# Performance work log

Hardware: AMD Instinct MI355X
Metric: run time of the kernel (lower is better)

Reference implementation:

```python
import jax, jax.numpy as jnp
import numpy as np

N_NODES = 50000
N_EDGES = 600000
N_GRAPHS = 100
IN_DIM, HID, OUT = 128, 128, 64
K = 2  # DGL TAGConv default hop count


def setup_inputs() -> dict:
    key = jax.random.key(0)
    ks = jax.random.split(key, 8)
    x = jax.random.normal(ks[0], (N_NODES, IN_DIM), dtype=jnp.float32)
    src = jax.random.randint(ks[1], (N_EDGES,), 0, N_NODES)
    dst = jax.random.randint(ks[2], (N_EDGES,), 0, N_NODES)
    graph_id = jnp.sort(jax.random.randint(ks[3], (N_NODES,), 0, N_GRAPHS))
    # TAGConv lin: Linear(in_feats*(K+1), out_feats), stored as (in*(K+1), out)
    W1 = jax.random.normal(ks[4], (IN_DIM * (K + 1), HID), dtype=jnp.float32) / np.sqrt(IN_DIM * (K + 1))
    b1 = jnp.zeros((HID,), dtype=jnp.float32)
    W2 = jax.random.normal(ks[5], (HID * (K + 1), OUT), dtype=jnp.float32) / np.sqrt(HID * (K + 1))
    b2 = jnp.zeros((OUT,), dtype=jnp.float32)
    return {"x": x, "W1": W1, "b1": b1, "W2": W2, "b2": b2,
            "src": src, "dst": dst, "graph_id": graph_id}


def _tagconv(h, src, dst, norm, W, b):
    """DGL TAGConv: relu(concat_k (D^-1/2 A D^-1/2)^k h @ W + b), k=0..K."""
    feats = [h]
    cur = h
    for _ in range(K):
        cur = cur * norm[:, None]
        cur = jax.ops.segment_sum(cur[src], dst, num_segments=N_NODES)
        cur = cur * norm[:, None]
        feats.append(cur)
    out = jnp.concatenate(feats, axis=-1) @ W + b
    return jax.nn.relu(out)


def reference(x, W1, b1, W2, b2, src, dst, graph_id):
    # symmetric norm from in-degrees (clamped to 1), as in DGL TAGConv
    deg = jax.ops.segment_sum(jnp.ones_like(dst, dtype=x.dtype), dst, num_segments=N_NODES)
    norm = jnp.clip(deg, 1.0, None) ** -0.5
    h = _tagconv(x, src, dst, norm, W1, b1)
    h = _tagconv(h, src, dst, norm, W2, b2)
    # MaxPooling readout: per-graph max over nodes
    return jax.ops.segment_max(h, graph_id, num_segments=N_GRAPHS)
```

## Files before the change

kernel.cpp:

```cpp
#include <hip/hip_runtime.h>
#include <hip/hip_bf16.h>

#define N_NODES 50000
#define N_EDGES 600000
#define N_GRAPHS 100
#define M_PAD 50176
#define TSLICE ((size_t)M_PAD * 32)

typedef __bf16 bf16_t;
typedef __attribute__((ext_vector_type(8))) __bf16 bf16x8;
typedef __attribute__((ext_vector_type(4))) __bf16 bf16x4;
typedef __attribute__((ext_vector_type(2))) __bf16 bf16x2;
typedef __attribute__((ext_vector_type(4))) float f32x4;

__global__ void degk(const int* __restrict__ dst, int* __restrict__ deg,
                     int* __restrict__ rank, int n) {
    int i = blockIdx.x * 256 + threadIdx.x;
    if (i < n) rank[i] = atomicAdd(&deg[dst[i]], 1);
}

__global__ __launch_bounds__(1024) void scan1(const int* __restrict__ deg,
                                              int* __restrict__ row_off,
                                              int* __restrict__ partial,
                                              float* __restrict__ norm, int n) {
    __shared__ int buf[1024];
    int i = blockIdx.x * 1024 + threadIdx.x;
    int v = (i < n) ? deg[i] : 0;
    buf[threadIdx.x] = v;
    __syncthreads();
    for (int off = 1; off < 1024; off <<= 1) {
        int t = (threadIdx.x >= off) ? buf[threadIdx.x - off] : 0;
        __syncthreads();
        buf[threadIdx.x] += t;
        __syncthreads();
    }
    if (i < n) {
        row_off[i + 1] = buf[threadIdx.x];
        float d = fmaxf((float)v, 1.0f);
        norm[i] = 1.0f / sqrtf(d);
    }
    if (threadIdx.x == 1023) partial[blockIdx.x] = buf[1023];
}

__global__ __launch_bounds__(256) void scan3(int* __restrict__ row_off,
                                             const int* __restrict__ partial, int n) {
    int i = blockIdx.x * 256 + threadIdx.x;
    int c = (blockIdx.x * 256) >> 10;
    __shared__ int pre;
    if (threadIdx.x < 64) {
        int v = (threadIdx.x < c) ? partial[threadIdx.x] : 0;
        for (int off = 32; off; off >>= 1) v += __shfl_down(v, off, 64);
        if (threadIdx.x == 0) pre = v;
    }
    __syncthreads();
    if (i == 0) row_off[0] = 0;
    if (i < n) row_off[i + 1] += pre;
}

#define NPRE 6250
#define NSC  ((N_EDGES + 255) / 256)
#define NPW  ((384 * 192 + 255) / 256)
__global__ __launch_bounds__(256) void midk(const float* __restrict__ x,
                                            const float* __restrict__ norm,
                                            bf16_t* __restrict__ xb, bf16_t* __restrict__ xs,
                                            const int* __restrict__ src, const int* __restrict__ dst,
                                            const int* __restrict__ row_off,
                                            const int* __restrict__ rank,
                                            int* __restrict__ csr_src,
                                            const float* __restrict__ W1, bf16_t* __restrict__ Wp1,
                                            const float* __restrict__ W2, bf16_t* __restrict__ Wp2) {
    int b = blockIdx.x;
    if (b < NPRE) {
        int i = b * 256 + threadIdx.x;
        int node = i >> 5, c4 = i & 31;
        float4 v = *(const float4*)(x + (size_t)node * 128 + c4 * 4);
        float nd = norm[node];
        bf16x4 ob, os;
        ob[0] = (bf16_t)v.x; ob[1] = (bf16_t)v.y; ob[2] = (bf16_t)v.z; ob[3] = (bf16_t)v.w;
        os[0] = (bf16_t)(v.x * nd); os[1] = (bf16_t)(v.y * nd);
        os[2] = (bf16_t)(v.z * nd); os[3] = (bf16_t)(v.w * nd);
        size_t t = (size_t)(c4 >> 3) * TSLICE + (size_t)node * 32 + (c4 & 7) * 4;
        *(bf16x4*)(xb + t) = ob;
        *(bf16x4*)(xs + t) = os;
    } else if (b < NPRE + NSC) {
        int e = (b - NPRE) * 256 + threadIdx.x;
        if (e >= N_EDGES) return;
        int d = dst[e];
        csr_src[row_off[d] + rank[e]] = src[e];
    } else {
        int i = (b - NPRE - NSC) * 256 + threadIdx.x;
        const float* W; bf16_t* Wp; int N; int idx;
        if (i < 384 * 128)                 { W = W1; Wp = Wp1; N = 128; idx = i; }
        else if (i < 384 * 128 + 384 * 64) { W = W2; Wp = Wp2; N = 64;  idx = i - 384 * 128; }
        else return;
        int k = idx / N, n = idx - k * N;
        int kt = k >> 5, q = (k >> 3) & 3, j = k & 7;
        int nt = n >> 4, ln = n & 15;
        int lane = q * 16 + ln;
        Wp[(((size_t)kt * (N >> 4) + nt) * 64 + lane) * 8 + j] = (bf16_t)W[idx];
    }
}

template <bool SCALED>
__global__ __launch_bounds__(256) void spmm_xcd(const bf16_t* __restrict__ in,
                                                bf16_t* __restrict__ out_c,
                                                bf16_t* __restrict__ out_s,
                                                const float* __restrict__ norm,
                                                const int* __restrict__ row_off,
                                                const int* __restrict__ csr_src, int n) {
    int bid  = blockIdx.x;
    int xcd  = bid & 7;
    int tile = xcd >> 1;
    int sub  = bid >> 3;
    int grp  = threadIdx.x >> 2;
    int l    = threadIdx.x & 3;
    int node = (sub * 2 + (xcd & 1)) * 64 + grp;
    if (node >= n) return;
    int e0 = row_off[node], e1 = row_off[node + 1];
    const bf16_t* base = in + (size_t)tile * TSLICE + l * 8;
    float acc[8] = {};
    int e = e0;
    for (; e + 8 <= e1; e += 8) {
        int s0 = csr_src[e + 0];
        int s1 = csr_src[e + 1];
        int s2 = csr_src[e + 2];
        int s3 = csr_src[e + 3];
        int s4 = csr_src[e + 4];
        int s5 = csr_src[e + 5];
        int s6 = csr_src[e + 6];
        int s7 = csr_src[e + 7];
        bf16x8 v0 = *(const bf16x8*)(base + (size_t)s0 * 32);
        bf16x8 v1 = *(const bf16x8*)(base + (size_t)s1 * 32);
        bf16x8 v2 = *(const bf16x8*)(base + (size_t)s2 * 32);
        bf16x8 v3 = *(const bf16x8*)(base + (size_t)s3 * 32);
        bf16x8 v4 = *(const bf16x8*)(base + (size_t)s4 * 32);
        bf16x8 v5 = *(const bf16x8*)(base + (size_t)s5 * 32);
        bf16x8 v6 = *(const bf16x8*)(base + (size_t)s6 * 32);
        bf16x8 v7 = *(const bf16x8*)(base + (size_t)s7 * 32);
#pragma unroll
        for (int j = 0; j < 8; j++)
            acc[j] += (((float)v0[j] + (float)v1[j]) + ((float)v2[j] + (float)v3[j]))
                    + (((float)v4[j] + (float)v5[j]) + ((float)v6[j] + (float)v7[j]));
    }
    if (e + 4 <= e1) {
        int s0 = csr_src[e + 0];
        int s1 = csr_src[e + 1];
        int s2 = csr_src[e + 2];
        int s3 = csr_src[e + 3];
        bf16x8 v0 = *(const bf16x8*)(base + (size_t)s0 * 32);
        bf16x8 v1 = *(const bf16x8*)(base + (size_t)s1 * 32);
        bf16x8 v2 = *(const bf16x8*)(base + (size_t)s2 * 32);
        bf16x8 v3 = *(const bf16x8*)(base + (size_t)s3 * 32);
#pragma unroll
        for (int j = 0; j < 8; j++)
            acc[j] += ((float)v0[j] + (float)v1[j]) + ((float)v2[j] + (float)v3[j]);
        e += 4;
    }
    for (; e < e1; e++) {
        int s = csr_src[e];
        bf16x8 v = *(const bf16x8*)(base + (size_t)s * 32);
#pragma unroll
        for (int j = 0; j < 8; j++) acc[j] += (float)v[j];
    }
    float nd = norm[node];
    bf16x8 oc, os;
#pragma unroll
    for (int j = 0; j < 8; j++) {
        float c = acc[j] * nd;
        oc[j] = (bf16_t)c;
        os[j] = (bf16_t)(c * nd);
    }
    size_t t = (size_t)tile * TSLICE + (size_t)node * 32 + l * 8;
    *(bf16x8*)(out_c + t) = oc;
    if (SCALED) *(bf16x8*)(out_s + t) = os;
}

template <int NT, bool LAYER1>
__global__ __launch_bounds__(256) void gemm_mfma(const bf16_t* __restrict__ f0,
                                                 const bf16_t* __restrict__ f1,
                                                 const bf16_t* __restrict__ f2,
                                                 const bf16_t* __restrict__ Wp,
                                                 const float* __restrict__ bias,
                                                 const float* __restrict__ norm,
                                                 bf16_t* __restrict__ out_b,
                                                 bf16_t* __restrict__ out_s,
                                                 float* __restrict__ out_f, int M) {
    int wave = threadIdx.x >> 6;
    int lane = threadIdx.x & 63;
    int q = lane >> 4, ln = lane & 15;
    int row0 = blockIdx.x * 128 + wave * 32;

    f32x4 acc[2][NT] = {};
    const bf16_t* feats[3] = {f0, f1, f2};
    const bf16x8* Wf = (const bf16x8*)Wp;

#pragma unroll
    for (int kc = 0; kc < 12; kc++) {
        const bf16_t* A = feats[kc >> 2] + (size_t)(kc & 3) * TSLICE + q * 8;
        bf16x8 a0 = *(const bf16x8*)(A + (size_t)(row0 + ln) * 32);
        bf16x8 a1 = *(const bf16x8*)(A + (size_t)(row0 + 16 + ln) * 32);
        const bf16x8* Bp = Wf + (size_t)kc * NT * 64 + lane;
#pragma unroll
        for (int nt = 0; nt < NT; nt++) {
            bf16x8 b = Bp[nt * 64];
            acc[0][nt] = __builtin_amdgcn_mfma_f32_16x16x32_bf16(a0, b, acc[0][nt], 0, 0, 0);
            acc[1][nt] = __builtin_amdgcn_mfma_f32_16x16x32_bf16(a1, b, acc[1][nt], 0, 0, 0);
        }
    }

    float bv[NT];
#pragma unroll
    for (int nt = 0; nt < NT; nt++) bv[nt] = bias[nt * 16 + ln];

#pragma unroll
    for (int mt = 0; mt < 2; mt++) {
#pragma unroll
        for (int r = 0; r < 4; r++) {
            int row = row0 + mt * 16 + q * 4 + r;
            if (row >= M) continue;
            float nd = LAYER1 ? norm[row] : 0.f;
#pragma unroll
            for (int nt = 0; nt < NT; nt++) {
                float val = fmaxf(acc[mt][nt][r] + bv[nt], 0.f);
                if (LAYER1) {
                    size_t t = (size_t)(nt >> 1) * TSLICE + (size_t)row * 32 + (nt & 1) * 16 + ln;
                    out_b[t] = (bf16_t)val;
                    out_s[t] = (bf16_t)(val * nd);
                } else {
                    out_f[(size_t)row * 64 + nt * 16 + ln] = val;
                }
            }
        }
    }
}

__global__ __launch_bounds__(256) void maxpool2(const float* __restrict__ hF,
                                                const int* __restrict__ gid,
                                                unsigned int* __restrict__ out, int n) {
    int wave = threadIdx.x >> 6;
    int lane = threadIdx.x & 63;
    int n0 = blockIdx.x * 256 + wave * 64;
    if (n0 >= n) return;
    int n1 = min(n0 + 64, n);
    int cur = gid[n0];
    float m = 0.f;
    int i = n0;
    for (; i + 4 <= n1; i += 4) {
        int g0 = gid[i + 0], g1 = gid[i + 1], g2 = gid[i + 2], g3 = gid[i + 3];
        float v0 = hF[(size_t)(i + 0) * 64 + lane];
        float v1 = hF[(size_t)(i + 1) * 64 + lane];
        float v2 = hF[(size_t)(i + 2) * 64 + lane];
        float v3 = hF[(size_t)(i + 3) * 64 + lane];
        if (g0 != cur) { atomicMax(&out[cur * 64 + lane], __float_as_uint(m)); cur = g0; m = v0; } else m = fmaxf(m, v0);
        if (g1 != cur) { atomicMax(&out[cur * 64 + lane], __float_as_uint(m)); cur = g1; m = v1; } else m = fmaxf(m, v1);
        if (g2 != cur) { atomicMax(&out[cur * 64 + lane], __float_as_uint(m)); cur = g2; m = v2; } else m = fmaxf(m, v2);
        if (g3 != cur) { atomicMax(&out[cur * 64 + lane], __float_as_uint(m)); cur = g3; m = v3; } else m = fmaxf(m, v3);
    }
    for (; i < n1; i++) {
        int g = gid[i];
        float v = hF[(size_t)i * 64 + lane];
        if (g != cur) { atomicMax(&out[cur * 64 + lane], __float_as_uint(m)); cur = g; m = v; }
        else m = fmaxf(m, v);
    }
    atomicMax(&out[cur * 64 + lane], __float_as_uint(m));
}

extern "C" void kernel_launch(void* const* d_in, const int* in_sizes, int n_in,
                              void* d_out, int out_size, void* d_ws, size_t ws_size,
                              hipStream_t stream) {
    const float* x  = (const float*)d_in[0];
    const float* W1 = (const float*)d_in[1];
    const float* b1 = (const float*)d_in[2];
    const float* W2 = (const float*)d_in[3];
    const float* b2 = (const float*)d_in[4];
    const int* src  = (const int*)d_in[5];
    const int* dst  = (const int*)d_in[6];
    const int* gid  = (const int*)d_in[7];
    float* out = (float*)d_out;

    char* ws = (char*)d_ws;
    size_t off = 0;
    auto take = [&](size_t bytes) {
        void* p = ws + off;
        off = (off + bytes + 255) & ~(size_t)255;
        return p;
    };
    int* deg     = (int*)take((size_t)N_NODES * 4);
    size_t zero_bytes = off;
    float* norm  = (float*)take((size_t)N_NODES * 4);
    int* row_off = (int*)take((size_t)(N_NODES + 1) * 4);
    int* partial = (int*)take(64 * 4);
    int* rank    = (int*)take((size_t)N_EDGES * 4);
    int* csr_src = (int*)take((size_t)N_EDGES * 4);
    bf16_t* Wp1  = (bf16_t*)take((size_t)384 * 128 * 2);
    bf16_t* Wp2  = (bf16_t*)take((size_t)384 * 64 * 2);
    bf16_t* B0 = (bf16_t*)take((size_t)M_PAD * 128 * 2);
    bf16_t* B1 = (bf16_t*)take((size_t)M_PAD * 128 * 2);
    bf16_t* B2 = (bf16_t*)take((size_t)M_PAD * 128 * 2);
    bf16_t* B3 = (bf16_t*)take((size_t)M_PAD * 128 * 2);
    bf16_t* B4 = (bf16_t*)take((size_t)M_PAD * 128 * 2);
    bf16_t* B5 = (bf16_t*)take((size_t)M_PAD * 128 * 2);
    (void)ws_size; (void)in_sizes; (void)n_in; (void)out_size;

    hipMemsetAsync(d_ws, 0, zero_bytes, stream);
    hipMemsetAsync(d_out, 0, (size_t)N_GRAPHS * 64 * 4, stream);

    degk<<<(N_EDGES + 255) / 256, 256, 0, stream>>>(dst, deg, rank, N_EDGES);
    int nchunks = (N_NODES + 1023) / 1024;
    scan1<<<nchunks, 1024, 0, stream>>>(deg, row_off, partial, norm, N_NODES);
    scan3<<<(N_NODES + 255) / 256, 256, 0, stream>>>(row_off, partial, N_NODES);
    midk<<<NPRE + NSC + NPW, 256, 0, stream>>>(x, norm, B0, B1, src, dst, row_off, rank,
                                               csr_src, W1, Wp1, W2, Wp2);

    int spmm_grid = 8 * 391;
    int gemm_grid = M_PAD / 128;

    spmm_xcd<true><<<spmm_grid, 256, 0, stream>>>(B1, B2, B4, norm, row_off, csr_src, N_NODES);
    spmm_xcd<false><<<spmm_grid, 256, 0, stream>>>(B4, B3, nullptr, norm, row_off, csr_src, N_NODES);
    gemm_mfma<8, true><<<gemm_grid, 256, 0, stream>>>(B0, B2, B3, Wp1, b1, norm, B5, B1, nullptr, N_NODES);
    spmm_xcd<true><<<spmm_grid, 256, 0, stream>>>(B1, B2, B4, norm, row_off, csr_src, N_NODES);
    spmm_xcd<false><<<spmm_grid, 256, 0, stream>>>(B4, B3, nullptr, norm, row_off, csr_src, N_NODES);
    gemm_mfma<4, false><<<gemm_grid, 256, 0, stream>>>(B5, B2, B3, Wp2, b2, nullptr, nullptr, nullptr, (float*)B0, N_NODES);
    maxpool2<<<(N_NODES + 255) / 256, 256, 0, stream>>>((const float*)B0, gid, (unsigned int*)out, N_NODES);
}
```

Baseline: 281.8 us.

## Apply layer-2 weights before propagation and split SpMM edges across thread halves

Layer 2 is reordered to multiply h by W2 first, since A(hW) = (Ah)W. The first propagation then runs on 128 projected columns, and the second hop only on the 64 columns that need two hops. The 64-wide results are summed with bias and ReLU inside the pooling kernel, which shrinks the gather traffic in layer-2 SpMM. SpMM now splits each node's edges between two 4-lane halves with a predicated first batch of 8 loads and a shuffle reduction, and stores through nontemporal writes. The cost is extra workspace buffers and a different bf16 rounding order.

```diff
diff --git a/kernel.cpp b/kernel.cpp
--- a/kernel.cpp
+++ b/kernel.cpp
@@ -10,7 +10,6 @@
 typedef __bf16 bf16_t;
 typedef __attribute__((ext_vector_type(8))) __bf16 bf16x8;
 typedef __attribute__((ext_vector_type(4))) __bf16 bf16x4;
-typedef __attribute__((ext_vector_type(2))) __bf16 bf16x2;
 typedef __attribute__((ext_vector_type(4))) float f32x4;
 
 __global__ void degk(const int* __restrict__ dst, int* __restrict__ deg,
@@ -89,108 +88,97 @@
         csr_src[row_off[d] + rank[e]] = src[e];
     } else {
         int i = (b - NPRE - NSC) * 256 + threadIdx.x;
-        const float* W; bf16_t* Wp; int N; int idx;
-        if (i < 384 * 128)                 { W = W1; Wp = Wp1; N = 128; idx = i; }
-        else if (i < 384 * 128 + 384 * 64) { W = W2; Wp = Wp2; N = 64;  idx = i - 384 * 128; }
-        else return;
-        int k = idx / N, n = idx - k * N;
-        int kt = k >> 5, q = (k >> 3) & 3, j = k & 7;
-        int nt = n >> 4, ln = n & 15;
-        int lane = q * 16 + ln;
-        Wp[(((size_t)kt * (N >> 4) + nt) * 64 + lane) * 8 + j] = (bf16_t)W[idx];
-    }
-}
-
-template <bool SCALED>
-__global__ __launch_bounds__(256) void spmm_xcd(const bf16_t* __restrict__ in,
-                                                bf16_t* __restrict__ out_c,
-                                                bf16_t* __restrict__ out_s,
-                                                const float* __restrict__ norm,
-                                                const int* __restrict__ row_off,
-                                                const int* __restrict__ csr_src, int n) {
+        if (i < 384 * 128) {
+            int k = i >> 7, n = i & 127;
+            int kt = k >> 5, q = (k >> 3) & 3, j = k & 7;
+            int nt = n >> 4, ln = n & 15;
+            Wp1[(((size_t)kt * 8 + nt) * 64 + q * 16 + ln) * 8 + j] = (bf16_t)W1[i];
+        } else if (i < 384 * 128 + 384 * 64) {
+            int idx = i - 384 * 128;
+            int k384 = idx >> 6, n = idx & 63;
+            int blk = k384 >> 7, kk = k384 & 127;
+            int col = blk * 64 + n;
+            int kt = kk >> 5, q = (kk >> 3) & 3, j = kk & 7;
+            int nt = col >> 4, ln = col & 15;
+            Wp2[(((size_t)kt * 12 + nt) * 64 + q * 16 + ln) * 8 + j] = (bf16_t)W2[idx];
+        }
+    }
+}
+
+template <int TILES, bool SCALED>
+__global__ __launch_bounds__(256) void spmm8(const bf16_t* __restrict__ in,
+                                             bf16_t* __restrict__ out_c,
+                                             bf16_t* __restrict__ out_s,
+                                             const float* __restrict__ norm,
+                                             const int* __restrict__ row_off,
+                                             const int* __restrict__ csr, int n) {
+    constexpr int PARTS = 8 / TILES;
     int bid  = blockIdx.x;
     int xcd  = bid & 7;
-    int tile = xcd >> 1;
+    int tile = xcd / PARTS;
+    int part = xcd % PARTS;
     int sub  = bid >> 3;
-    int grp  = threadIdx.x >> 2;
+    int grp  = threadIdx.x >> 3;
+    int half = (threadIdx.x >> 2) & 1;
     int l    = threadIdx.x & 3;
-    int node = (sub * 2 + (xcd & 1)) * 64 + grp;
+    int node = (sub * PARTS + part) * 32 + grp;
     if (node >= n) return;
     int e0 = row_off[node], e1 = row_off[node + 1];
     const bf16_t* base = in + (size_t)tile * TSLICE + l * 8;
     float acc[8] = {};
-    int e = e0;
-    for (; e + 8 <= e1; e += 8) {
-        int s0 = csr_src[e + 0];
-        int s1 = csr_src[e + 1];
-        int s2 = csr_src[e + 2];
-        int s3 = csr_src[e + 3];
-        int s4 = csr_src[e + 4];
-        int s5 = csr_src[e + 5];
-        int s6 = csr_src[e + 6];
-        int s7 = csr_src[e + 7];
-        bf16x8 v0 = *(const bf16x8*)(base + (size_t)s0 * 32);
-        bf16x8 v1 = *(const bf16x8*)(base + (size_t)s1 * 32);
-        bf16x8 v2 = *(const bf16x8*)(base + (size_t)s2 * 32);
-        bf16x8 v3 = *(const bf16x8*)(base + (size_t)s3 * 32);
-        bf16x8 v4 = *(const bf16x8*)(base + (size_t)s4 * 32);
-        bf16x8 v5 = *(const bf16x8*)(base + (size_t)s5 * 32);
-        bf16x8 v6 = *(const bf16x8*)(base + (size_t)s6 * 32);
-        bf16x8 v7 = *(const bf16x8*)(base + (size_t)s7 * 32);
-#pragma unroll
-        for (int j = 0; j < 8; j++)
-            acc[j] += (((float)v0[j] + (float)v1[j]) + ((float)v2[j] + (float)v3[j]))
-                    + (((float)v4[j] + (float)v5[j]) + ((float)v6[j] + (float)v7[j]));
-    }
-    if (e + 4 <= e1) {
-        int s0 = csr_src[e + 0];
-        int s1 = csr_src[e + 1];
-        int s2 = csr_src[e + 2];
-        int s3 = csr_src[e + 3];
-        bf16x8 v0 = *(const bf16x8*)(base + (size_t)s0 * 32);
-        bf16x8 v1 = *(const bf16x8*)(base + (size_t)s1 * 32);
-        bf16x8 v2 = *(const bf16x8*)(base + (size_t)s2 * 32);
-        bf16x8 v3 = *(const bf16x8*)(base + (size_t)s3 * 32);
-#pragma unroll
-        for (int j = 0; j < 8; j++)
-            acc[j] += ((float)v0[j] + (float)v1[j]) + ((float)v2[j] + (float)v3[j]);
-        e += 4;
-    }
-    for (; e < e1; e++) {
-        int s = csr_src[e];
-        bf16x8 v = *(const bf16x8*)(base + (size_t)s * 32);
-#pragma unroll
-        for (int j = 0; j < 8; j++) acc[j] += (float)v[j];
-    }
+    if (e0 < e1) {
+        int be   = e0 + half;
+        int cnt  = (e1 - be + 1) >> 1;
+        int emax = e1 - 1;
+        int s[8];
+#pragma unroll
+        for (int k = 0; k < 8; k++) s[k] = csr[min(be + 2 * k, emax)];
+        bf16x8 v[8];
+#pragma unroll
+        for (int k = 0; k < 8; k++) v[k] = *(const bf16x8*)(base + (size_t)s[k] * 32);
+#pragma unroll
+        for (int k = 0; k < 8; k++) {
+            float wk = (k < cnt) ? 1.0f : 0.0f;
+#pragma unroll
+            for (int j = 0; j < 8; j++) acc[j] += wk * (float)v[k][j];
+        }
+        for (int e = be + 16; e < e1; e += 2) {
+            int ss = csr[e];
+            bf16x8 vv = *(const bf16x8*)(base + (size_t)ss * 32);
+#pragma unroll
+            for (int j = 0; j < 8; j++) acc[j] += (float)vv[j];
+        }
+    }
+#pragma unroll
+    for (int j = 0; j < 8; j++) acc[j] += __shfl_xor(acc[j], 4, 64);
     float nd = norm[node];
-    bf16x8 oc, os;
-#pragma unroll
-    for (int j = 0; j < 8; j++) {
-        float c = acc[j] * nd;
-        oc[j] = (bf16_t)c;
-        os[j] = (bf16_t)(c * nd);
-    }
     size_t t = (size_t)tile * TSLICE + (size_t)node * 32 + l * 8;
-    *(bf16x8*)(out_c + t) = oc;
-    if (SCALED) *(bf16x8*)(out_s + t) = os;
-}
-
-template <int NT, bool LAYER1>
-__global__ __launch_bounds__(256) void gemm_mfma(const bf16_t* __restrict__ f0,
-                                                 const bf16_t* __restrict__ f1,
-                                                 const bf16_t* __restrict__ f2,
-                                                 const bf16_t* __restrict__ Wp,
-                                                 const float* __restrict__ bias,
-                                                 const float* __restrict__ norm,
-                                                 bf16_t* __restrict__ out_b,
-                                                 bf16_t* __restrict__ out_s,
-                                                 float* __restrict__ out_f, int M) {
+    if (half == 0) {
+        bf16x8 oc;
+#pragma unroll
+        for (int j = 0; j < 8; j++) oc[j] = (bf16_t)(acc[j] * nd);
+        __builtin_nontemporal_store(oc, (bf16x8*)(out_c + t));
+    } else if (SCALED) {
+        float n2 = nd * nd;
+        bf16x8 os;
+#pragma unroll
+        for (int j = 0; j < 8; j++) os[j] = (bf16_t)(acc[j] * n2);
+        __builtin_nontemporal_store(os, (bf16x8*)(out_s + t));
+    }
+}
+
+__global__ __launch_bounds__(256) void gemm1k(const bf16_t* __restrict__ f0,
+                                              const bf16_t* __restrict__ f1,
+                                              const bf16_t* __restrict__ f2,
+                                              const bf16_t* __restrict__ Wp,
+                                              const float* __restrict__ bias,
+                                              bf16_t* __restrict__ outb, int M) {
     int wave = threadIdx.x >> 6;
     int lane = threadIdx.x & 63;
     int q = lane >> 4, ln = lane & 15;
     int row0 = blockIdx.x * 128 + wave * 32;
 
-    f32x4 acc[2][NT] = {};
+    f32x4 acc[2][8] = {};
     const bf16_t* feats[3] = {f0, f1, f2};
     const bf16x8* Wf = (const bf16x8*)Wp;
 
@@ -199,18 +187,18 @@
         const bf16_t* A = feats[kc >> 2] + (size_t)(kc & 3) * TSLICE + q * 8;
         bf16x8 a0 = *(const bf16x8*)(A + (size_t)(row0 + ln) * 32);
         bf16x8 a1 = *(const bf16x8*)(A + (size_t)(row0 + 16 + ln) * 32);
-        const bf16x8* Bp = Wf + (size_t)kc * NT * 64 + lane;
-#pragma unroll
-        for (int nt = 0; nt < NT; nt++) {
+        const bf16x8* Bp = Wf + (size_t)kc * 8 * 64 + lane;
+#pragma unroll
+        for (int nt = 0; nt < 8; nt++) {
             bf16x8 b = Bp[nt * 64];
             acc[0][nt] = __builtin_amdgcn_mfma_f32_16x16x32_bf16(a0, b, acc[0][nt], 0, 0, 0);
             acc[1][nt] = __builtin_amdgcn_mfma_f32_16x16x32_bf16(a1, b, acc[1][nt], 0, 0, 0);
         }
     }
 
-    float bv[NT];
-#pragma unroll
-    for (int nt = 0; nt < NT; nt++) bv[nt] = bias[nt * 16 + ln];
+    float bv[8];
+#pragma unroll
+    for (int nt = 0; nt < 8; nt++) bv[nt] = bias[nt * 16 + ln];
 
 #pragma unroll
     for (int mt = 0; mt < 2; mt++) {
@@ -218,47 +206,86 @@
         for (int r = 0; r < 4; r++) {
             int row = row0 + mt * 16 + q * 4 + r;
             if (row >= M) continue;
-            float nd = LAYER1 ? norm[row] : 0.f;
-#pragma unroll
-            for (int nt = 0; nt < NT; nt++) {
+#pragma unroll
+            for (int nt = 0; nt < 8; nt++) {
                 float val = fmaxf(acc[mt][nt][r] + bv[nt], 0.f);
-                if (LAYER1) {
-                    size_t t = (size_t)(nt >> 1) * TSLICE + (size_t)row * 32 + (nt & 1) * 16 + ln;
-                    out_b[t] = (bf16_t)val;
-                    out_s[t] = (bf16_t)(val * nd);
-                } else {
-                    out_f[(size_t)row * 64 + nt * 16 + ln] = val;
-                }
+                outb[(size_t)(nt >> 1) * TSLICE + (size_t)row * 32 + (nt & 1) * 16 + ln] = (bf16_t)val;
             }
         }
     }
 }
 
-__global__ __launch_bounds__(256) void maxpool2(const float* __restrict__ hF,
-                                                const int* __restrict__ gid,
-                                                unsigned int* __restrict__ out, int n) {
+__global__ __launch_bounds__(256) void gemm2k(const bf16_t* __restrict__ h,
+                                              const bf16_t* __restrict__ Wp,
+                                              const float* __restrict__ bias,
+                                              const float* __restrict__ norm,
+                                              float* __restrict__ t0,
+                                              bf16_t* __restrict__ uvs, int M) {
+    int wave = threadIdx.x >> 6;
+    int lane = threadIdx.x & 63;
+    int q = lane >> 4, ln = lane & 15;
+    int row0 = blockIdx.x * 128 + wave * 32;
+
+    f32x4 acc[2][12] = {};
+    const bf16x8* Wf = (const bf16x8*)Wp;
+
+#pragma unroll
+    for (int kc = 0; kc < 4; kc++) {
+        const bf16_t* A = h + (size_t)kc * TSLICE + q * 8;
+        bf16x8 a0 = *(const bf16x8*)(A + (size_t)(row0 + ln) * 32);
+        bf16x8 a1 = *(const bf16x8*)(A + (size_t)(row0 + 16 + ln) * 32);
+        const bf16x8* Bp = Wf + (size_t)kc * 12 * 64 + lane;
+#pragma unroll
+        for (int nt = 0; nt < 12; nt++) {
+            bf16x8 b = Bp[nt * 64];
+            acc[0][nt] = __builtin_amdgcn_mfma_f32_16x16x32_bf16(a0, b, acc[0][nt], 0, 0, 0);
+            acc[1][nt] = __builtin_amdgcn_mfma_f32_16x16x32_bf16(a1, b, acc[1][nt], 0, 0, 0);
+        }
+    }
+
+    float bv[4];
+#pragma unroll
+    for (int nt = 0; nt < 4; nt++) bv[nt] = bias[nt * 16 + ln];
+
+#pragma unroll
+    for (int mt = 0; mt < 2; mt++) {
+#pragma unroll
+        for (int r = 0; r < 4; r++) {
+            int row = row0 + mt * 16 + q * 4 + r;
+            if (row >= M) continue;
+            float nd = norm[row];
+#pragma unroll
+            for (int nt = 0; nt < 4; nt++)
+                __builtin_nontemporal_store(acc[mt][nt][r] + bv[nt],
+                                            t0 + (size_t)row * 64 + nt * 16 + ln);
+#pragma unroll
+            for (int nt = 4; nt < 12; nt++) {
+                int col = (nt - 4) * 16 + ln;
+                uvs[(size_t)(col >> 5) * TSLICE + (size_t)row * 32 + (col & 31)] =
+                    (bf16_t)(acc[mt][nt][r] * nd);
+            }
+        }
+    }
+}
+
+__global__ __launch_bounds__(256) void finpool(const float* __restrict__ t0,
+                                               const bf16_t* __restrict__ Au,
+                                               const bf16_t* __restrict__ A2v,
+                                               const int* __restrict__ gid,
+                                               unsigned int* __restrict__ out, int n) {
     int wave = threadIdx.x >> 6;
     int lane = threadIdx.x & 63;
     int n0 = blockIdx.x * 256 + wave * 64;
     if (n0 >= n) return;
     int n1 = min(n0 + 64, n);
+    size_t cb = (size_t)(lane >> 5) * TSLICE + (lane & 31);
     int cur = gid[n0];
     float m = 0.f;
-    int i = n0;
-    for (; i + 4 <= n1; i += 4) {
-        int g0 = gid[i + 0], g1 = gid[i + 1], g2 = gid[i + 2], g3 = gid[i + 3];
-        float v0 = hF[(size_t)(i + 0) * 64 + lane];
-        float v1 = hF[(size_t)(i + 1) * 64 + lane];
-        float v2 = hF[(size_t)(i + 2) * 64 + lane];
-        float v3 = hF[(size_t)(i + 3) * 64 + lane];
-        if (g0 != cur) { atomicMax(&out[cur * 64 + lane], __float_as_uint(m)); cur = g0; m = v0; } else m = fmaxf(m, v0);
-        if (g1 != cur) { atomicMax(&out[cur * 64 + lane], __float_as_uint(m)); cur = g1; m = v1; } else m = fmaxf(m, v1);
-        if (g2 != cur) { atomicMax(&out[cur * 64 + lane], __float_as_uint(m)); cur = g2; m = v2; } else m = fmaxf(m, v2);
-        if (g3 != cur) { atomicMax(&out[cur * 64 + lane], __float_as_uint(m)); cur = g3; m = v3; } else m = fmaxf(m, v3);
-    }
-    for (; i < n1; i++) {
+    for (int i = n0; i < n1; i++) {
         int g = gid[i];
-        float v = hF[(size_t)i * 64 + lane];
+        float v = fmaxf(t0[(size_t)i * 64 + lane]
+                        + (float)Au[cb + (size_t)i * 32]
+                        + (float)A2v[cb + (size_t)i * 32], 0.f);
         if (g != cur) { atomicMax(&out[cur * 64 + lane], __float_as_uint(m)); cur = g; m = v; }
         else m = fmaxf(m, v);
     }
@@ -300,6 +327,11 @@
     bf16_t* B3 = (bf16_t*)take((size_t)M_PAD * 128 * 2);
     bf16_t* B4 = (bf16_t*)take((size_t)M_PAD * 128 * 2);
     bf16_t* B5 = (bf16_t*)take((size_t)M_PAD * 128 * 2);
+    float*  B6 = (float*)take((size_t)M_PAD * 64 * 4);
+    bf16_t* B7 = (bf16_t*)take((size_t)M_PAD * 128 * 2);
+    bf16_t* B8 = (bf16_t*)take((size_t)M_PAD * 128 * 2);
+    bf16_t* B9 = (bf16_t*)take((size_t)M_PAD * 128 * 2);
+    bf16_t* B10= (bf16_t*)take((size_t)M_PAD * 128 * 2);
     (void)ws_size; (void)in_sizes; (void)n_in; (void)out_size;
 
     hipMemsetAsync(d_ws, 0, zero_bytes, stream);
@@ -312,14 +344,15 @@
     midk<<<NPRE + NSC + NPW, 256, 0, stream>>>(x, norm, B0, B1, src, dst, row_off, rank,
                                                csr_src, W1, Wp1, W2, Wp2);
 
-    int spmm_grid = 8 * 391;
+    int grid4 = 8 * ((N_NODES + 63) / 64);
+    int grid2 = 8 * ((N_NODES + 127) / 128);
     int gemm_grid = M_PAD / 128;
 
-    spmm_xcd<true><<<spmm_grid, 256, 0, stream>>>(B1, B2, B4, norm, row_off, csr_src, N_NODES);
-    spmm_xcd<false><<<spmm_grid, 256, 0, stream>>>(B4, B3, nullptr, norm, row_off, csr_src, N_NODES);
-    gemm_mfma<8, true><<<gemm_grid, 256, 0, stream>>>(B0, B2, B3, Wp1, b1, norm, B5, B1, nullptr, N_NODES);
-    spmm_xcd<true><<<spmm_grid, 256, 0, stream>>>(B1, B2, B4, norm, row_off, csr_src, N_NODES);
-    spmm_xcd<false><<<spmm_grid, 256, 0, stream>>>(B4, B3, nullptr, norm, row_off, csr_src, N_NODES);
-    gemm_mfma<4, false><<<gemm_grid, 256, 0, stream>>>(B5, B2, B3, Wp2, b2, nullptr, nullptr, nullptr, (float*)B0, N_NODES);
-    maxpool2<<<(N_NODES + 255) / 256, 256, 0, stream>>>((const float*)B0, gid, (unsigned int*)out, N_NODES);
-}
+    spmm8<4, true ><<<grid4, 256, 0, stream>>>(B1, B2, B3, norm, row_off, csr_src, N_NODES);
+    spmm8<4, false><<<grid4, 256, 0, stream>>>(B3, B4, nullptr, norm, row_off, csr_src, N_NODES);
+    gemm1k<<<gemm_grid, 256, 0, stream>>>(B0, B2, B4, Wp1, b1, B5, N_NODES);
+    gemm2k<<<gemm_grid, 256, 0, stream>>>(B5, Wp2, b2, norm, B6, B7, N_NODES);
+    spmm8<4, true ><<<grid4, 256, 0, stream>>>(B7, B8, B9, norm, row_off, csr_src, N_NODES);
+    spmm8<2, false><<<grid2, 256, 0, stream>>>(B9 + 2 * TSLICE, B10, nullptr, norm, row_off, csr_src, N_NODES);
+    finpool<<<(N_NODES + 255) / 256, 256, 0, stream>>>(B6, B8, B10, gid, (unsigned int*)out, N_NODES);
+}
```

New measurement: 284.2 us. No clear change (+0.8%).
